# Performance work log

Measured on AMD Instinct MI355X. Metric: run time of the kernel, lower is better.

The kernel has to match this reference:

```python
import jax, jax.numpy as jnp
import numpy as np

B, S, DIN, DOUT = 4, 2048, 4096, 4096
QMAX = 127  # 2**(8-1) - 1


def setup_inputs() -> dict:
    key = jax.random.key(0)
    k_x, k_w, k_b, k_ws = jax.random.split(key, 4)
    x = jax.random.normal(k_x, (B, S, DIN), dtype=jnp.float32)
    # int8-valued weights stored as int32 (as in the torch module's .int() weight)
    weight = jax.random.randint(k_w, (DOUT, DIN), -QMAX, QMAX + 1, dtype=jnp.int32)
    bias = jax.random.randint(k_b, (DOUT,), -10, 11, dtype=jnp.int32)
    # per-input-channel weight scale, shape (out_features, 1)
    weight_scale = (jax.random.uniform(k_ws, (DOUT, 1), dtype=jnp.float32) * 0.01 + 1e-4)
    input_scale = jnp.float32(0.02)
    output_scale = jnp.float32(0.05)
    return {
        "x": x,
        "weight": weight,
        "bias": bias,
        "weight_scale": weight_scale,
        "input_scale": input_scale,
        "output_scale": output_scale,
    }


def reference(x, weight, bias, weight_scale, input_scale, output_scale):
    # fake-quantize activations: round to int grid, then dequantize back to float
    xq = jnp.round(x / input_scale).astype(jnp.int32).astype(jnp.float32) * input_scale
    # dequantize weights: (O, I)
    w = weight.astype(jnp.float32) * weight_scale
    # fp32 GEMM: [B,S,I] x [I,O] -> [B,S,O]
    ret = jnp.einsum("bsi,oi->bso", xq, w)
    ret = ret + bias.astype(jnp.float32)
    # requantize output to int grid (int32 output, as in torch .int())
    return jnp.round(ret / output_scale).astype(jnp.int32)
```

## Files before the change

### kernel.cpp

```cpp
#include <hip/hip_runtime.h>
#include <stdint.h>

#define MDIM 8192
#define KDIM 4096
#define NDIM 4096
#define BK   64
#define NKT  (KDIM / BK)

typedef float f32x4 __attribute__((ext_vector_type(4)));
typedef _Float16 h16x8 __attribute__((ext_vector_type(8)));
typedef float fl4 __attribute__((ext_vector_type(4)));
typedef int i32x4 __attribute__((ext_vector_type(4)));

__device__ __forceinline__ void gload_lds16(const void* g, void* l) {
    __builtin_amdgcn_global_load_lds(
        (__attribute__((address_space(1))) void*)(uintptr_t)g,
        (__attribute__((address_space(3))) void*)(uintptr_t)l,
        16, 0, 0);
}

__global__ void __launch_bounds__(256) quant_kernel(const float* __restrict__ x,
                                                    short* __restrict__ xq,
                                                    const int* __restrict__ w,
                                                    short* __restrict__ wq,
                                                    const float* __restrict__ p_is) {
    if (blockIdx.x < 2048) {
        const float inv_is = 1.0f / p_is[0];
        const int64_t stride = (int64_t)2048 * 256 * 8;
        for (int64_t i = ((int64_t)blockIdx.x * 256 + threadIdx.x) * 8;
             i < (int64_t)MDIM * KDIM; i += stride) {
            fl4 a = __builtin_nontemporal_load((const fl4*)(x + i));
            fl4 b = __builtin_nontemporal_load((const fl4*)(x + i + 4));
            h16x8 o;
            o[0] = (_Float16)rintf(a[0] * inv_is);
            o[1] = (_Float16)rintf(a[1] * inv_is);
            o[2] = (_Float16)rintf(a[2] * inv_is);
            o[3] = (_Float16)rintf(a[3] * inv_is);
            o[4] = (_Float16)rintf(b[0] * inv_is);
            o[5] = (_Float16)rintf(b[1] * inv_is);
            o[6] = (_Float16)rintf(b[2] * inv_is);
            o[7] = (_Float16)rintf(b[3] * inv_is);
            *(h16x8*)(xq + i) = o;
        }
    } else {
        const int64_t stride = (int64_t)1024 * 256 * 8;
        for (int64_t i = (((int64_t)blockIdx.x - 2048) * 256 + threadIdx.x) * 8;
             i < (int64_t)NDIM * KDIM; i += stride) {
            i32x4 a = *(const i32x4*)(w + i);
            i32x4 b = *(const i32x4*)(w + i + 4);
            h16x8 o;
            o[0] = (_Float16)(float)a[0];
            o[1] = (_Float16)(float)a[1];
            o[2] = (_Float16)(float)a[2];
            o[3] = (_Float16)(float)a[3];
            o[4] = (_Float16)(float)b[0];
            o[5] = (_Float16)(float)b[1];
            o[6] = (_Float16)(float)b[2];
            o[7] = (_Float16)(float)b[3];
            *(h16x8*)(wq + i) = o;
        }
    }
}


#define PH_MID() do { \
    __builtin_amdgcn_s_barrier(); \
    asm volatile("s_waitcnt lgkmcnt(0)" ::: "memory"); \
    __builtin_amdgcn_sched_barrier(0); \
    __builtin_amdgcn_s_setprio(1); \
  } while (0)

#define PH_END() do { \
    __builtin_amdgcn_s_setprio(0); \
    __builtin_amdgcn_s_barrier(); \
    __builtin_amdgcn_sched_barrier(0); \
  } while (0)

#define PH_END_VM6() do { \
    __builtin_amdgcn_s_setprio(0); \
    asm volatile("s_waitcnt vmcnt(6)" ::: "memory"); \
    __builtin_amdgcn_s_barrier(); \
    __builtin_amdgcn_sched_barrier(0); \
  } while (0)

__global__ void __launch_bounds__(512, 2) gemm_f16_kernel(
    const short* __restrict__ A,
    const short* __restrict__ Bw,
    const int* __restrict__ bias,
    const float* __restrict__ wscale,
    const float* __restrict__ p_is,
    const float* __restrict__ p_os,
    int* __restrict__ out) {
    __shared__ __align__(16) short lds[65536];

    const int tid  = threadIdx.x;
    const int lane = tid & 63;
    const int wave = tid >> 6;
    const int quad = lane >> 4;
    const int r16  = lane & 15;
    const int sw   = r16 & 7;

    const int flat  = blockIdx.y * gridDim.x + blockIdx.x;
    const int wgid  = (flat & 7) * 64 + (flat >> 3);
    const int m_blk = wgid >> 4;
    const int n_blk = wgid & 15;
    const int m0 = m_blk * 256;
    const int n0 = n_blk * 256;

    const int wmi = wave >> 2;
    const int wni = wave & 3;

    const int srow = tid >> 3;
    const int skc  = (tid & 7) ^ (srow & 7);
    const short* gA = A  + (int64_t)(m0 + srow) * KDIM + skc * 8;
    const short* gB = Bw + (int64_t)(n0 + srow) * KDIM + skc * 8;

#define STAGE_A(b, ha, T) do { \
    const short* _g = gA + (int64_t)((ha) * 128) * KDIM + (T) * BK; \
    gload_lds16(_g,             &lds[(b)*16384 + (ha)*8192 + wave*512]); \
    gload_lds16(_g + 64*KDIM,   &lds[(b)*16384 + (ha)*8192 + 4096 + wave*512]); \
  } while (0)
#define STAGE_B(b, ha, T) do { \
    const short* _g = gB + (int64_t)((ha) * 128) * KDIM + (T) * BK; \
    gload_lds16(_g,             &lds[32768 + (b)*16384 + (ha)*8192 + wave*512]); \
    gload_lds16(_g + 64*KDIM,   &lds[32768 + (b)*16384 + (ha)*8192 + 4096 + wave*512]); \
  } while (0)

    const int aRowOff = (wmi * 128 + r16) * 64;
    const int bRowOff = 32768 + (wni * 64 + r16) * 64;
    const int cOff0   = (quad ^ sw) * 8;
    const int cOff1   = cOff0 ^ 32;

#define LDA(b, mh, mi, ks) \
    (*(const h16x8*)&lds[(b)*16384 + aRowOff + ((mh)*64 + (mi)*16)*64 + ((ks) ? cOff1 : cOff0)])
#define LDB(b, nh, nj, ks) \
    (*(const h16x8*)&lds[(b)*16384 + bRowOff + ((nh)*32 + (nj)*16)*64 + ((ks) ? cOff1 : cOff0)])

#define READ_A(b, mh) do { \
    _Pragma("unroll") for (int mi = 0; mi < 4; ++mi) { \
        aR[mi][0] = LDA(b, mh, mi, 0); aR[mi][1] = LDA(b, mh, mi, 1); } \
  } while (0)
#define READ_B(b, nh, dst) do { \
    _Pragma("unroll") for (int nj = 0; nj < 2; ++nj) { \
        dst[nj][0] = LDB(b, nh, nj, 0); dst[nj][1] = LDB(b, nh, nj, 1); } \
  } while (0)
#define MFMA_Q(mh, nh, bsrc) do { \
    _Pragma("unroll") for (int mi = 0; mi < 4; ++mi) \
    _Pragma("unroll") for (int nj = 0; nj < 2; ++nj) \
    _Pragma("unroll") for (int ks = 0; ks < 2; ++ks) \
        acc[(mh)*4 + mi][(nh)*2 + nj] = __builtin_amdgcn_mfma_f32_16x16x32_f16( \
            aR[mi][ks], bsrc[nj][ks], acc[(mh)*4 + mi][(nh)*2 + nj], 0, 0, 0); \
  } while (0)

    f32x4 acc[8][4];
#pragma unroll
    for (int i = 0; i < 8; ++i)
#pragma unroll
        for (int j = 0; j < 4; ++j) acc[i][j] = (f32x4)0.0f;

    h16x8 aR[4][2], bLo[2][2], bHi[2][2];

    STAGE_B(0, 0, 0);  STAGE_B(0, 1, 0);
    STAGE_A(0, 0, 0);  STAGE_A(0, 1, 0);
    STAGE_B(1, 0, 1);  STAGE_B(1, 1, 1);
    STAGE_A(1, 0, 1);
    asm volatile("s_waitcnt vmcnt(6)" ::: "memory");
    __builtin_amdgcn_s_barrier();
    __builtin_amdgcn_sched_barrier(0);

    for (int it = 0; it < NKT / 2; ++it) {
        const int t1 = 2 * it + 1;
        const int tA = (2 * it + 2) & (NKT - 1);
        const int tB = (2 * it + 3) & (NKT - 1);

        READ_A(0, 0); READ_B(0, 0, bLo);
        STAGE_A(1, 1, t1);
        asm volatile("s_waitcnt lgkmcnt(8)" ::: "memory");
        PH_MID(); MFMA_Q(0, 0, bLo); PH_END();
        READ_B(0, 1, bHi);
        PH_MID(); MFMA_Q(0, 1, bHi); PH_END();
        READ_A(0, 1);
        STAGE_B(0, 0, tA);
        PH_MID(); MFMA_Q(1, 1, bHi); PH_END();
        STAGE_B(0, 1, tA);
        STAGE_A(0, 0, tA);
        PH_MID(); MFMA_Q(1, 0, bLo); PH_END_VM6();
        READ_A(1, 0); READ_B(1, 0, bLo);
        STAGE_A(0, 1, tA);
        asm volatile("s_waitcnt lgkmcnt(8)" ::: "memory");
        PH_MID(); MFMA_Q(0, 0, bLo); PH_END();
        READ_B(1, 1, bHi);
        PH_MID(); MFMA_Q(0, 1, bHi); PH_END();
        READ_A(1, 1);
        STAGE_B(1, 0, tB);
        PH_MID(); MFMA_Q(1, 1, bHi); PH_END();
        STAGE_B(1, 1, tB);
        STAGE_A(1, 0, tB);
        PH_MID(); MFMA_Q(1, 0, bLo); PH_END_VM6();
    }

    const float is = p_is[0];
    const float inv_os = 1.0f / p_os[0];
    const int colBase = n0 + wni * 64;

    float alpha[4], beta[4];
#pragma unroll
    for (int nj = 0; nj < 4; ++nj) {
        const int col = colBase + nj * 16 + r16;
        alpha[nj] = is * wscale[col] * inv_os;
        beta[nj]  = (float)bias[col] * inv_os;
    }

#pragma unroll
    for (int mi = 0; mi < 8; ++mi) {
        const int row0 = m0 + wmi * 128 + mi * 16 + quad * 4;
#pragma unroll
        for (int nj = 0; nj < 4; ++nj) {
            const int col = colBase + nj * 16 + r16;
#pragma unroll
            for (int reg = 0; reg < 4; ++reg) {
                const float v = acc[mi][nj][reg] * alpha[nj] + beta[nj];
                __builtin_nontemporal_store(__float2int_rn(v),
                                            out + (int64_t)(row0 + reg) * NDIM + col);
            }
        }
    }
}

extern "C" void kernel_launch(void* const* d_in, const int* in_sizes, int n_in,
                              void* d_out, int out_size, void* d_ws, size_t ws_size,
                              hipStream_t stream) {
    (void)in_sizes; (void)n_in; (void)out_size; (void)ws_size;
    const float* x      = (const float*)d_in[0];
    const int*   weight = (const int*)d_in[1];
    const int*   bias   = (const int*)d_in[2];
    const float* wscale = (const float*)d_in[3];
    const float* p_is   = (const float*)d_in[4];
    const float* p_os   = (const float*)d_in[5];

    short* xq = (short*)d_ws;
    short* wq = xq + (size_t)MDIM * KDIM;

    quant_kernel<<<3072, 256, 0, stream>>>(x, xq, weight, wq, p_is);

    dim3 grid(NDIM / 256, MDIM / 256);
    gemm_f16_kernel<<<grid, 512, 0, stream>>>(xq, wq, bias, wscale, p_is, p_os, (int*)d_out);
}
```

Before: 479.9 us.

## Drop explicit LDS waitcnts in GEMM phases and widen quant kernel per-thread work

Removes the manual s_waitcnt lgkmcnt(0)/lgkmcnt(8) and the sched_barrier inside PH_MID, so the compiler's own dependency tracking decides when LDS reads must complete before each MFMA quarter. The quant prepass now handles 16 elements per thread per iteration instead of 8, issuing more loads in flight. Dropping the sched_barrier lets the compiler move LDS reads and MFMAs across the barrier/setprio boundary, which may change the interleaving the phase schedule was designed around. Correctness then depends on the compiler inserting the required waits.

```diff
diff --git a/kernel.cpp b/kernel.cpp
--- a/kernel.cpp
+++ b/kernel.cpp
@@ -26,38 +26,60 @@
                                                     const float* __restrict__ p_is) {
     if (blockIdx.x < 2048) {
         const float inv_is = 1.0f / p_is[0];
-        const int64_t stride = (int64_t)2048 * 256 * 8;
-        for (int64_t i = ((int64_t)blockIdx.x * 256 + threadIdx.x) * 8;
+        const int64_t stride = (int64_t)2048 * 256 * 16;
+        for (int64_t i = ((int64_t)blockIdx.x * 256 + threadIdx.x) * 16;
              i < (int64_t)MDIM * KDIM; i += stride) {
             fl4 a = __builtin_nontemporal_load((const fl4*)(x + i));
             fl4 b = __builtin_nontemporal_load((const fl4*)(x + i + 4));
-            h16x8 o;
-            o[0] = (_Float16)rintf(a[0] * inv_is);
-            o[1] = (_Float16)rintf(a[1] * inv_is);
-            o[2] = (_Float16)rintf(a[2] * inv_is);
-            o[3] = (_Float16)rintf(a[3] * inv_is);
-            o[4] = (_Float16)rintf(b[0] * inv_is);
-            o[5] = (_Float16)rintf(b[1] * inv_is);
-            o[6] = (_Float16)rintf(b[2] * inv_is);
-            o[7] = (_Float16)rintf(b[3] * inv_is);
-            *(h16x8*)(xq + i) = o;
+            fl4 c = __builtin_nontemporal_load((const fl4*)(x + i + 8));
+            fl4 d = __builtin_nontemporal_load((const fl4*)(x + i + 12));
+            h16x8 o0, o1;
+            o0[0] = (_Float16)rintf(a[0] * inv_is);
+            o0[1] = (_Float16)rintf(a[1] * inv_is);
+            o0[2] = (_Float16)rintf(a[2] * inv_is);
+            o0[3] = (_Float16)rintf(a[3] * inv_is);
+            o0[4] = (_Float16)rintf(b[0] * inv_is);
+            o0[5] = (_Float16)rintf(b[1] * inv_is);
+            o0[6] = (_Float16)rintf(b[2] * inv_is);
+            o0[7] = (_Float16)rintf(b[3] * inv_is);
+            o1[0] = (_Float16)rintf(c[0] * inv_is);
+            o1[1] = (_Float16)rintf(c[1] * inv_is);
+            o1[2] = (_Float16)rintf(c[2] * inv_is);
+            o1[3] = (_Float16)rintf(c[3] * inv_is);
+            o1[4] = (_Float16)rintf(d[0] * inv_is);
+            o1[5] = (_Float16)rintf(d[1] * inv_is);
+            o1[6] = (_Float16)rintf(d[2] * inv_is);
+            o1[7] = (_Float16)rintf(d[3] * inv_is);
+            *(h16x8*)(xq + i)     = o0;
+            *(h16x8*)(xq + i + 8) = o1;
         }
     } else {
-        const int64_t stride = (int64_t)1024 * 256 * 8;
-        for (int64_t i = (((int64_t)blockIdx.x - 2048) * 256 + threadIdx.x) * 8;
+        const int64_t stride = (int64_t)1024 * 256 * 16;
+        for (int64_t i = (((int64_t)blockIdx.x - 2048) * 256 + threadIdx.x) * 16;
              i < (int64_t)NDIM * KDIM; i += stride) {
             i32x4 a = *(const i32x4*)(w + i);
             i32x4 b = *(const i32x4*)(w + i + 4);
-            h16x8 o;
-            o[0] = (_Float16)(float)a[0];
-            o[1] = (_Float16)(float)a[1];
-            o[2] = (_Float16)(float)a[2];
-            o[3] = (_Float16)(float)a[3];
-            o[4] = (_Float16)(float)b[0];
-            o[5] = (_Float16)(float)b[1];
-            o[6] = (_Float16)(float)b[2];
-            o[7] = (_Float16)(float)b[3];
-            *(h16x8*)(wq + i) = o;
+            i32x4 c = *(const i32x4*)(w + i + 8);
+            i32x4 d = *(const i32x4*)(w + i + 12);
+            h16x8 o0, o1;
+            o0[0] = (_Float16)(float)a[0];
+            o0[1] = (_Float16)(float)a[1];
+            o0[2] = (_Float16)(float)a[2];
+            o0[3] = (_Float16)(float)a[3];
+            o0[4] = (_Float16)(float)b[0];
+            o0[5] = (_Float16)(float)b[1];
+            o0[6] = (_Float16)(float)b[2];
+            o0[7] = (_Float16)(float)b[3];
+            o1[0] = (_Float16)(float)c[0];
+            o1[1] = (_Float16)(float)c[1];
+            o1[2] = (_Float16)(float)c[2];
+            o1[3] = (_Float16)(float)c[3];
+            o1[4] = (_Float16)(float)d[0];
+            o1[5] = (_Float16)(float)d[1];
+            o1[6] = (_Float16)(float)d[2];
+            o1[7] = (_Float16)(float)d[3];
+            *(h16x8*)(wq + i)     = o0;
+            *(h16x8*)(wq + i + 8) = o1;
         }
     }
 }
@@ -65,8 +87,6 @@
 
 #define PH_MID() do { \
     __builtin_amdgcn_s_barrier(); \
-    asm volatile("s_waitcnt lgkmcnt(0)" ::: "memory"); \
-    __builtin_amdgcn_sched_barrier(0); \
     __builtin_amdgcn_s_setprio(1); \
   } while (0)
 
@@ -175,7 +195,6 @@
 
         READ_A(0, 0); READ_B(0, 0, bLo);
         STAGE_A(1, 1, t1);
-        asm volatile("s_waitcnt lgkmcnt(8)" ::: "memory");
         PH_MID(); MFMA_Q(0, 0, bLo); PH_END();
         READ_B(0, 1, bHi);
         PH_MID(); MFMA_Q(0, 1, bHi); PH_END();
@@ -187,7 +206,6 @@
         PH_MID(); MFMA_Q(1, 0, bLo); PH_END_VM6();
         READ_A(1, 0); READ_B(1, 0, bLo);
         STAGE_A(0, 1, tA);
-        asm volatile("s_waitcnt lgkmcnt(8)" ::: "memory");
         PH_MID(); MFMA_Q(0, 0, bLo); PH_END();
         READ_B(1, 1, bHi);
         PH_MID(); MFMA_Q(0, 1, bHi); PH_END();
```

Result: slower. 493.1 us (+2.7%).

## Remap waves to 4x2 grid with 64x128 per-wave tiles and restructured pipeline

Applied to the files above, without the earlier changes.

Changes the wave layout from 2x4 (128x64 per wave) to 4x2 (64x128 per wave), so each wave loads its A fragments once per k-tile and streams four B quarter-groups. The main loop is rewritten as a TILE macro that interleaves LDS reads of the next B group with MFMAs on the current one, and issues whole-tile global-to-LDS stages at fixed points. The vmcnt wait threshold moves from 6 to 8 to match the new staging order. This aims to cut LDS read traffic for A and improve read/compute overlap. In exchange it changes the prefetch timing, which could expose global-load latency or barrier stalls.

```diff
diff --git a/kernel.cpp b/kernel.cpp
--- a/kernel.cpp
+++ b/kernel.cpp
@@ -76,9 +76,9 @@
     __builtin_amdgcn_sched_barrier(0); \
   } while (0)
 
-#define PH_END_VM6() do { \
+#define PH_END_VM8() do { \
     __builtin_amdgcn_s_setprio(0); \
-    asm volatile("s_waitcnt vmcnt(6)" ::: "memory"); \
+    asm volatile("s_waitcnt vmcnt(8)" ::: "memory"); \
     __builtin_amdgcn_s_barrier(); \
     __builtin_amdgcn_sched_barrier(0); \
   } while (0)
@@ -107,8 +107,8 @@
     const int m0 = m_blk * 256;
     const int n0 = n_blk * 256;
 
-    const int wmi = wave >> 2;
-    const int wni = wave & 3;
+    const int wmi = wave >> 1;
+    const int wni = wave & 1;
 
     const int srow = tid >> 3;
     const int skc  = (tid & 7) ^ (srow & 7);
@@ -126,96 +126,94 @@
     gload_lds16(_g + 64*KDIM,   &lds[32768 + (b)*16384 + (ha)*8192 + 4096 + wave*512]); \
   } while (0)
 
-    const int aRowOff = (wmi * 128 + r16) * 64;
-    const int bRowOff = 32768 + (wni * 64 + r16) * 64;
+    const int aRowOff = (wmi * 64 + r16) * 64;
+    const int bRowOff = 32768 + (wni * 128 + r16) * 64;
     const int cOff0   = (quad ^ sw) * 8;
     const int cOff1   = cOff0 ^ 32;
 
-#define LDA(b, mh, mi, ks) \
-    (*(const h16x8*)&lds[(b)*16384 + aRowOff + ((mh)*64 + (mi)*16)*64 + ((ks) ? cOff1 : cOff0)])
-#define LDB(b, nh, nj, ks) \
-    (*(const h16x8*)&lds[(b)*16384 + bRowOff + ((nh)*32 + (nj)*16)*64 + ((ks) ? cOff1 : cOff0)])
-
-#define READ_A(b, mh) do { \
+#define LDA(b, mi, ks) \
+    (*(const h16x8*)&lds[(b)*16384 + aRowOff + (mi)*1024 + ((ks) ? cOff1 : cOff0)])
+#define LDB(b, nj, ks) \
+    (*(const h16x8*)&lds[(b)*16384 + bRowOff + (nj)*1024 + ((ks) ? cOff1 : cOff0)])
+
+#define READ_A(b) do { \
     _Pragma("unroll") for (int mi = 0; mi < 4; ++mi) { \
-        aR[mi][0] = LDA(b, mh, mi, 0); aR[mi][1] = LDA(b, mh, mi, 1); } \
-  } while (0)
-#define READ_B(b, nh, dst) do { \
+        aR[mi][0] = LDA(b, mi, 0); aR[mi][1] = LDA(b, mi, 1); } \
+  } while (0)
+#define READ_BQ(b, q, dst) do { \
     _Pragma("unroll") for (int nj = 0; nj < 2; ++nj) { \
-        dst[nj][0] = LDB(b, nh, nj, 0); dst[nj][1] = LDB(b, nh, nj, 1); } \
-  } while (0)
-#define MFMA_Q(mh, nh, bsrc) do { \
+        dst[nj][0] = LDB(b, 2*(q) + nj, 0); dst[nj][1] = LDB(b, 2*(q) + nj, 1); } \
+  } while (0)
+#define MFMA_Q(q, bsrc) do { \
     _Pragma("unroll") for (int mi = 0; mi < 4; ++mi) \
     _Pragma("unroll") for (int nj = 0; nj < 2; ++nj) \
     _Pragma("unroll") for (int ks = 0; ks < 2; ++ks) \
-        acc[(mh)*4 + mi][(nh)*2 + nj] = __builtin_amdgcn_mfma_f32_16x16x32_f16( \
-            aR[mi][ks], bsrc[nj][ks], acc[(mh)*4 + mi][(nh)*2 + nj], 0, 0, 0); \
-  } while (0)
-
-    f32x4 acc[8][4];
-#pragma unroll
-    for (int i = 0; i < 8; ++i)
-#pragma unroll
-        for (int j = 0; j < 4; ++j) acc[i][j] = (f32x4)0.0f;
-
-    h16x8 aR[4][2], bLo[2][2], bHi[2][2];
-
-    STAGE_B(0, 0, 0);  STAGE_B(0, 1, 0);
-    STAGE_A(0, 0, 0);  STAGE_A(0, 1, 0);
-    STAGE_B(1, 0, 1);  STAGE_B(1, 1, 1);
-    STAGE_A(1, 0, 1);
-    asm volatile("s_waitcnt vmcnt(6)" ::: "memory");
+        acc[mi][2*(q) + nj] = __builtin_amdgcn_mfma_f32_16x16x32_f16( \
+            aR[mi][ks], bsrc[nj][ks], acc[mi][2*(q) + nj], 0, 0, 0); \
+  } while (0)
+
+    f32x4 acc[4][8];
+#pragma unroll
+    for (int i = 0; i < 4; ++i)
+#pragma unroll
+        for (int j = 0; j < 8; ++j) acc[i][j] = (f32x4)0.0f;
+
+    h16x8 aR[4][2], bG0[2][2], bG1[2][2];
+
+#define TILE(b, T2) do { \
+     \
+    READ_A(b); READ_BQ(b, 0, bG0); \
+    asm volatile("s_waitcnt lgkmcnt(8)" ::: "memory"); \
+    PH_MID(); \
+    READ_BQ(b, 1, bG1);             \
+    MFMA_Q(0, bG0); \
+    PH_END(); \
+     \
+    STAGE_A(b, 0, T2); STAGE_A(b, 1, T2); \
+    PH_MID(); \
+    READ_BQ(b, 2, bG0);             \
+    MFMA_Q(1, bG1); \
+    PH_END(); \
+     \
+    READ_BQ(b, 3, bG1); \
+    PH_MID(); \
+    MFMA_Q(2, bG0); \
+    PH_END(); \
+     \
+    STAGE_B(b, 0, T2); STAGE_B(b, 1, T2); \
+    PH_MID(); \
+    MFMA_Q(3, bG1); \
+    PH_END_VM8();                   \
+  } while (0)
+
+    STAGE_A(0, 0, 0); STAGE_A(0, 1, 0); STAGE_B(0, 0, 0); STAGE_B(0, 1, 0);
+    STAGE_A(1, 0, 1); STAGE_A(1, 1, 1); STAGE_B(1, 0, 1); STAGE_B(1, 1, 1);
+    asm volatile("s_waitcnt vmcnt(8)" ::: "memory");
     __builtin_amdgcn_s_barrier();
     __builtin_amdgcn_sched_barrier(0);
 
     for (int it = 0; it < NKT / 2; ++it) {
-        const int t1 = 2 * it + 1;
-        const int tA = (2 * it + 2) & (NKT - 1);
-        const int tB = (2 * it + 3) & (NKT - 1);
-
-        READ_A(0, 0); READ_B(0, 0, bLo);
-        STAGE_A(1, 1, t1);
-        asm volatile("s_waitcnt lgkmcnt(8)" ::: "memory");
-        PH_MID(); MFMA_Q(0, 0, bLo); PH_END();
-        READ_B(0, 1, bHi);
-        PH_MID(); MFMA_Q(0, 1, bHi); PH_END();
-        READ_A(0, 1);
-        STAGE_B(0, 0, tA);
-        PH_MID(); MFMA_Q(1, 1, bHi); PH_END();
-        STAGE_B(0, 1, tA);
-        STAGE_A(0, 0, tA);
-        PH_MID(); MFMA_Q(1, 0, bLo); PH_END_VM6();
-        READ_A(1, 0); READ_B(1, 0, bLo);
-        STAGE_A(0, 1, tA);
-        asm volatile("s_waitcnt lgkmcnt(8)" ::: "memory");
-        PH_MID(); MFMA_Q(0, 0, bLo); PH_END();
-        READ_B(1, 1, bHi);
-        PH_MID(); MFMA_Q(0, 1, bHi); PH_END();
-        READ_A(1, 1);
-        STAGE_B(1, 0, tB);
-        PH_MID(); MFMA_Q(1, 1, bHi); PH_END();
-        STAGE_B(1, 1, tB);
-        STAGE_A(1, 0, tB);
-        PH_MID(); MFMA_Q(1, 0, bLo); PH_END_VM6();
+        TILE(0, (2 * it + 2) & (NKT - 1));
+        TILE(1, (2 * it + 3) & (NKT - 1));
     }
 
     const float is = p_is[0];
     const float inv_os = 1.0f / p_os[0];
-    const int colBase = n0 + wni * 64;
-
-    float alpha[4], beta[4];
-#pragma unroll
-    for (int nj = 0; nj < 4; ++nj) {
+    const int colBase = n0 + wni * 128;
+
+    float alpha[8], beta[8];
+#pragma unroll
+    for (int nj = 0; nj < 8; ++nj) {
         const int col = colBase + nj * 16 + r16;
         alpha[nj] = is * wscale[col] * inv_os;
         beta[nj]  = (float)bias[col] * inv_os;
     }
 
 #pragma unroll
-    for (int mi = 0; mi < 8; ++mi) {
-        const int row0 = m0 + wmi * 128 + mi * 16 + quad * 4;
-#pragma unroll
-        for (int nj = 0; nj < 4; ++nj) {
+    for (int mi = 0; mi < 4; ++mi) {
+        const int row0 = m0 + wmi * 64 + mi * 16 + quad * 4;
+#pragma unroll
+        for (int nj = 0; nj < 8; ++nj) {
             const int col = colBase + nj * 16 + r16;
 #pragma unroll
             for (int reg = 0; reg < 4; ++reg) {
```

New measurement: 483.6 us. About the same (+0.8%).

## Switch GEMM inner loop from 16x16x32 to 32x32x16 f16 MFMA tiles

Applied to the files above, without the earlier changes.

Replaces the 16x16x32 MFMA instructions with 32x32x16 ones, restructuring the per-wave register fragments, LDS read offsets, phase schedule and epilogue output mapping to match. Larger MFMA tiles mean fewer LDS fragment reads per FLOP and fewer instructions issued. The cost is longer per-instruction latency and a different LDS access pattern, where the XOR swizzle may now cause bank conflicts, while the accumulator register count stays the same.

```diff
diff --git a/kernel.cpp b/kernel.cpp
--- a/kernel.cpp
+++ b/kernel.cpp
@@ -8,6 +8,7 @@
 #define NKT  (KDIM / BK)
 
 typedef float f32x4 __attribute__((ext_vector_type(4)));
+typedef float f32x16 __attribute__((ext_vector_type(16)));
 typedef _Float16 h16x8 __attribute__((ext_vector_type(8)));
 typedef float fl4 __attribute__((ext_vector_type(4)));
 typedef int i32x4 __attribute__((ext_vector_type(4)));
@@ -96,9 +97,9 @@
     const int tid  = threadIdx.x;
     const int lane = tid & 63;
     const int wave = tid >> 6;
-    const int quad = lane >> 4;
-    const int r16  = lane & 15;
-    const int sw   = r16 & 7;
+    const int c31  = lane & 31;
+    const int h    = lane >> 5;
+    const int sw7  = lane & 7;
 
     const int flat  = blockIdx.y * gridDim.x + blockIdx.x;
     const int wgid  = (flat & 7) * 64 + (flat >> 3);
@@ -126,39 +127,54 @@
     gload_lds16(_g + 64*KDIM,   &lds[32768 + (b)*16384 + (ha)*8192 + 4096 + wave*512]); \
   } while (0)
 
-    const int aRowOff = (wmi * 128 + r16) * 64;
-    const int bRowOff = 32768 + (wni * 64 + r16) * 64;
-    const int cOff0   = (quad ^ sw) * 8;
-    const int cOff1   = cOff0 ^ 32;
-
-#define LDA(b, mh, mi, ks) \
-    (*(const h16x8*)&lds[(b)*16384 + aRowOff + ((mh)*64 + (mi)*16)*64 + ((ks) ? cOff1 : cOff0)])
-#define LDB(b, nh, nj, ks) \
-    (*(const h16x8*)&lds[(b)*16384 + bRowOff + ((nh)*32 + (nj)*16)*64 + ((ks) ? cOff1 : cOff0)])
-
-#define READ_A(b, mh) do { \
-    _Pragma("unroll") for (int mi = 0; mi < 4; ++mi) { \
-        aR[mi][0] = LDA(b, mh, mi, 0); aR[mi][1] = LDA(b, mh, mi, 1); } \
-  } while (0)
-#define READ_B(b, nh, dst) do { \
-    _Pragma("unroll") for (int nj = 0; nj < 2; ++nj) { \
-        dst[nj][0] = LDB(b, nh, nj, 0); dst[nj][1] = LDB(b, nh, nj, 1); } \
-  } while (0)
-#define MFMA_Q(mh, nh, bsrc) do { \
-    _Pragma("unroll") for (int mi = 0; mi < 4; ++mi) \
-    _Pragma("unroll") for (int nj = 0; nj < 2; ++nj) \
-    _Pragma("unroll") for (int ks = 0; ks < 2; ++ks) \
-        acc[(mh)*4 + mi][(nh)*2 + nj] = __builtin_amdgcn_mfma_f32_16x16x32_f16( \
-            aR[mi][ks], bsrc[nj][ks], acc[(mh)*4 + mi][(nh)*2 + nj], 0, 0, 0); \
-  } while (0)
-
-    f32x4 acc[8][4];
-#pragma unroll
-    for (int i = 0; i < 8; ++i)
-#pragma unroll
-        for (int j = 0; j < 4; ++j) acc[i][j] = (f32x4)0.0f;
-
-    h16x8 aR[4][2], bLo[2][2], bHi[2][2];
+    const int aRow0 = (wmi * 128 + c31) * 64;
+    const int bRow0 = 32768 + (wni * 64 + c31) * 64;
+    int cof[4];
+#pragma unroll
+    for (int ks = 0; ks < 4; ++ks) cof[ks] = ((ks * 2 + h) ^ sw7) * 8;
+
+#define LDA32(b, mb, ks) (*(const h16x8*)&lds[(b)*16384 + aRow0 + (mb)*2048 + cof[ks]])
+#define LDB32(b, nb, ks) (*(const h16x8*)&lds[(b)*16384 + bRow0 + (nb)*2048 + cof[ks]])
+
+    f32x16 acc[4][2];
+#pragma unroll
+    for (int i = 0; i < 4; ++i)
+#pragma unroll
+        for (int j = 0; j < 2; ++j) acc[i][j] = (f32x16)0.0f;
+
+    h16x8 aR[2][4], bN0[4], bN1[4];
+
+#define MFMA_PAIR(mbBase, nb, bsrc) do { \
+    _Pragma("unroll") for (int ks = 0; ks < 4; ++ks) \
+        acc[(mbBase)][nb] = __builtin_amdgcn_mfma_f32_32x32x16_f16( \
+            aR[0][ks], bsrc[ks], acc[(mbBase)][nb], 0, 0, 0); \
+    _Pragma("unroll") for (int ks = 0; ks < 4; ++ks) \
+        acc[(mbBase) + 1][nb] = __builtin_amdgcn_mfma_f32_32x32x16_f16( \
+            aR[1][ks], bsrc[ks], acc[(mbBase) + 1][nb], 0, 0, 0); \
+  } while (0)
+
+#define TILE(b, To, Ts) do { \
+     \
+    _Pragma("unroll") for (int ks = 0; ks < 4; ++ks) { \
+        aR[0][ks] = LDA32(b, 0, ks); aR[1][ks] = LDA32(b, 1, ks); } \
+    _Pragma("unroll") for (int ks = 0; ks < 4; ++ks) bN0[ks] = LDB32(b, 0, ks); \
+    STAGE_A((b) ^ 1, 1, To); \
+    asm volatile("s_waitcnt lgkmcnt(8)" ::: "memory"); \
+    PH_MID(); MFMA_PAIR(0, 0, bN0); PH_END(); \
+     \
+    _Pragma("unroll") for (int ks = 0; ks < 4; ++ks) bN1[ks] = LDB32(b, 1, ks); \
+    PH_MID(); MFMA_PAIR(0, 1, bN1); PH_END(); \
+     \
+    _Pragma("unroll") for (int ks = 0; ks < 4; ++ks) { \
+        aR[0][ks] = LDA32(b, 2, ks); aR[1][ks] = LDA32(b, 3, ks); } \
+    STAGE_B(b, 0, Ts); \
+    asm volatile("s_waitcnt lgkmcnt(8)" ::: "memory"); \
+    PH_MID(); MFMA_PAIR(2, 1, bN1); PH_END(); \
+     \
+    STAGE_B(b, 1, Ts); \
+    STAGE_A(b, 0, Ts); \
+    PH_MID(); MFMA_PAIR(2, 0, bN0); PH_END_VM6(); \
+  } while (0)
 
     STAGE_B(0, 0, 0);  STAGE_B(0, 1, 0);
     STAGE_A(0, 0, 0);  STAGE_A(0, 1, 0);
@@ -169,59 +185,36 @@
     __builtin_amdgcn_sched_barrier(0);
 
     for (int it = 0; it < NKT / 2; ++it) {
-        const int t1 = 2 * it + 1;
-        const int tA = (2 * it + 2) & (NKT - 1);
-        const int tB = (2 * it + 3) & (NKT - 1);
-
-        READ_A(0, 0); READ_B(0, 0, bLo);
-        STAGE_A(1, 1, t1);
-        asm volatile("s_waitcnt lgkmcnt(8)" ::: "memory");
-        PH_MID(); MFMA_Q(0, 0, bLo); PH_END();
-        READ_B(0, 1, bHi);
-        PH_MID(); MFMA_Q(0, 1, bHi); PH_END();
-        READ_A(0, 1);
-        STAGE_B(0, 0, tA);
-        PH_MID(); MFMA_Q(1, 1, bHi); PH_END();
-        STAGE_B(0, 1, tA);
-        STAGE_A(0, 0, tA);
-        PH_MID(); MFMA_Q(1, 0, bLo); PH_END_VM6();
-        READ_A(1, 0); READ_B(1, 0, bLo);
-        STAGE_A(0, 1, tA);
-        asm volatile("s_waitcnt lgkmcnt(8)" ::: "memory");
-        PH_MID(); MFMA_Q(0, 0, bLo); PH_END();
-        READ_B(1, 1, bHi);
-        PH_MID(); MFMA_Q(0, 1, bHi); PH_END();
-        READ_A(1, 1);
-        STAGE_B(1, 0, tB);
-        PH_MID(); MFMA_Q(1, 1, bHi); PH_END();
-        STAGE_B(1, 1, tB);
-        STAGE_A(1, 0, tB);
-        PH_MID(); MFMA_Q(1, 0, bLo); PH_END_VM6();
+        TILE(0, 2 * it + 1, (2 * it + 2) & (NKT - 1));
+        TILE(1, (2 * it + 2) & (NKT - 1), (2 * it + 3) & (NKT - 1));
     }
 
     const float is = p_is[0];
     const float inv_os = 1.0f / p_os[0];
     const int colBase = n0 + wni * 64;
 
-    float alpha[4], beta[4];
-#pragma unroll
-    for (int nj = 0; nj < 4; ++nj) {
-        const int col = colBase + nj * 16 + r16;
-        alpha[nj] = is * wscale[col] * inv_os;
-        beta[nj]  = (float)bias[col] * inv_os;
-    }
-
-#pragma unroll
-    for (int mi = 0; mi < 8; ++mi) {
-        const int row0 = m0 + wmi * 128 + mi * 16 + quad * 4;
-#pragma unroll
-        for (int nj = 0; nj < 4; ++nj) {
-            const int col = colBase + nj * 16 + r16;
-#pragma unroll
-            for (int reg = 0; reg < 4; ++reg) {
-                const float v = acc[mi][nj][reg] * alpha[nj] + beta[nj];
-                __builtin_nontemporal_store(__float2int_rn(v),
-                                            out + (int64_t)(row0 + reg) * NDIM + col);
+    float alpha[2], beta[2];
+#pragma unroll
+    for (int nb = 0; nb < 2; ++nb) {
+        const int col = colBase + nb * 32 + c31;
+        alpha[nb] = is * wscale[col] * inv_os;
+        beta[nb]  = (float)bias[col] * inv_os;
+    }
+
+#pragma unroll
+    for (int mb = 0; mb < 4; ++mb) {
+#pragma unroll
+        for (int nb = 0; nb < 2; ++nb) {
+            const int col = colBase + nb * 32 + c31;
+#pragma unroll
+            for (int g = 0; g < 4; ++g) {
+#pragma unroll
+                for (int j = 0; j < 4; ++j) {
+                    const int row = m0 + wmi * 128 + mb * 32 + j + g * 8 + h * 4;
+                    const float v = acc[mb][nb][g * 4 + j] * alpha[nb] + beta[nb];
+                    __builtin_nontemporal_store(__float2int_rn(v),
+                                                out + (int64_t)row * NDIM + col);
+                }
             }
         }
     }
```

Result: slower. 496.4 us (+3.4%).
